# Kernel tuning notes

Hardware: AMD Instinct MI355X
Metric: run time of the kernel (lower is better)

## Reference

```python
import jax, jax.numpy as jnp
import numpy as np

NODE_N = 23
SEQ_LEN = 35
N_HEADS = 3
BN_EPS = 1e-5


def _normalize_digraph(A):
    # column-normalize: A @ diag(1/deg) (st-gcn tools.normalize_digraph)
    Dl = A.sum(0)
    inv = np.where(Dl > 0, 1.0 / np.where(Dl > 0, Dl, 1.0), 0.0)
    return A * inv[None, :]


def _build_A_ske():
    n = NODE_N
    bone = [[0, 2], [1, 2], [0, 3], [3, 6], [6, 9], [1, 4], [4, 7], [7, 10],
            [2, 5], [5, 8], [8, 12], [12, 15], [15, 17], [17, 19], [19, 21],
            [8, 13], [13, 16], [16, 18], [18, 20], [20, 22], [8, 11], [11, 14]]
    A_in = np.zeros((n, n), np.float64)
    A_out = np.zeros((n, n), np.float64)
    for i, j in bone:
        A_in[i, j] = 1.0
        A_out[j, i] = 1.0
    A_self = np.eye(n, dtype=np.float64)
    return np.stack([_normalize_digraph(A_in), _normalize_digraph(A_out), A_self]).astype(np.float32)


def setup_inputs() -> dict:
    key = jax.random.key(0)
    ks = jax.random.split(key, 12)
    b, c, o, n, l = 256, 64, 64, NODE_N, SEQ_LEN
    stdv = 1.0 / np.sqrt(n)           # reset_parameters: 1/sqrt(att.size(2)) = 1/sqrt(n)
    cbound = 1.0 / np.sqrt(c)         # conv2d 1x1 default init bound (fan_in = in_c)
    u = lambda k, shape, bnd: jax.random.uniform(k, shape, jnp.float32, -bnd, bnd)
    return {
        "x": jax.random.normal(ks[0], (b, c, n, l), jnp.float32),
        "cw1": u(ks[1], (N_HEADS, o, c), cbound),
        "cb1": u(ks[2], (N_HEADS, o), cbound),
        "cw2": u(ks[3], (N_HEADS, o, c), cbound),
        "cb2": u(ks[4], (N_HEADS, o), cbound),
        "bn_gamma": jnp.ones((N_HEADS, n * n), jnp.float32),
        "bn_beta": jnp.zeros((N_HEADS, n * n), jnp.float32),
        "mw": u(ks[5], (N_HEADS, o, c), cbound),
        "mb": u(ks[6], (N_HEADS, o), cbound),
        "att": jnp.full((N_HEADS, n, n), 1e-6, jnp.float32),
        "A_ske": jnp.asarray(_build_A_ske()),
        "weight_seq": u(ks[7], (l, l), stdv),
        "bias": u(ks[8], (l,), stdv),
    }


def reference(x, cw1, cb1, cw2, cb2, bn_gamma, bn_beta, mw, mb, att, A_ske, weight_seq, bias):
    b, c, n, l = x.shape
    o = cw1.shape[1]
    xp = jnp.transpose(x, (0, 1, 3, 2))                      # [b,c,l,n]

    # --- A_adp heads (vectorized across 3 heads) ---
    o1 = jnp.einsum('hoc,bcln->bholn', cw1, xp) + cb1[None, :, :, None, None]
    o2 = jnp.einsum('hoc,bcln->bholn', cw2, xp) + cb2[None, :, :, None, None]
    o1 = o1.reshape(b, N_HEADS, o * l, n)
    o2 = o2.reshape(b, N_HEADS, o * l, n)
    att_m = jnp.einsum('bhkm,bhkn->bhmn', o2, o1) / (o * l)  # [b,3,n,n]

    # BatchNorm1d over flattened n*n features, batch statistics (training mode)
    flat = att_m.reshape(b, N_HEADS, n * n)
    mean = flat.mean(axis=0)                                  # [3,n*n]
    var = flat.var(axis=0)                                    # biased, as torch BN
    flat = (flat - mean) / jnp.sqrt(var + BN_EPS) * bn_gamma + bn_beta
    A_adp = jax.nn.softmax(flat.reshape(b, N_HEADS, n, n), axis=-2)
    # dropout is identity in eval mode

    # --- graph convolution per head ---
    A = A_ske[None] + att[None] + A_adp                       # [b,3,n,n]
    support = jnp.einsum('bcln,bhnm->bhclm', xp, A)           # [b,3,c,l,n]
    head = jnp.einsum('hoc,bhclm->bholm', mw, support) + mb[None, :, :, None, None]
    gcn = jnp.transpose(head.sum(axis=1), (0, 1, 3, 2))       # [b,o,n,l]

    out = jnp.einsum('bonl,lm->bonm', gcn, weight_seq) + bias
    return out
```

## Files before the change

### kernel.cpp

```cpp
#include <hip/hip_runtime.h>
#include <hip/hip_bf16.h>

typedef __hip_bfloat16 bf16;
typedef __attribute__((ext_vector_type(8))) short bf16x8;
typedef __attribute__((ext_vector_type(4))) float f32x4;
typedef __attribute__((ext_vector_type(4))) unsigned short us4;
typedef __attribute__((ext_vector_type(8))) unsigned short us8;

#define NB   256
#define NN   23
#define NL   35
#define NNL  805
#define CNL  51520
#define NSQ  529
#define HF   1587
#define NCN  1472

#define OFF_W     0
#define OFF_U1    12288
#define OFF_U2    12480
#define OFF_S     12672
#define OFF_ATTM  12800
#define OFF_MEAN  419072
#define OFF_RSTD  420672
#define OFF_A     422272
#define OFF_MWH   828544
#define OFF_MWL   834688
#define OFF_MBS   840832
#define OFF_XTB   840960

__device__ inline unsigned short bfh(float x) {
    unsigned u = __float_as_uint(x);
    return (unsigned short)((u + 0x7FFFu + ((u >> 16) & 1u)) >> 16);
}
__device__ inline float bfh2f(unsigned short h) {
    return __uint_as_float(((unsigned)h) << 16);
}
__device__ inline unsigned short bf16rn(float x) {
    __hip_bfloat16 h = __float2bfloat16(x);
    return __builtin_bit_cast(unsigned short, h);
}

__global__ __launch_bounds__(512) void k_xt(const float* __restrict__ x,
                                            float* __restrict__ ws) {
    int b = blockIdx.x, ch = blockIdx.y, t = threadIdx.x;
    __shared__ float sx[16 * 805];
    const float* xb = x + b * CNL + ch * (16 * 805);
    unsigned short* xo = (unsigned short*)(ws + OFF_XTB) + (size_t)b * NL * 2944;
    for (int i = t; i < 16 * 805; i += 512) sx[i] = xb[i];
    __syncthreads();
    for (int item = t; item < 35 * 46; item += 512) {
        int l = item / 46, rem = item - l * 46;
        int n = rem >> 1, k2 = rem & 1;
        us8 hi, lo;
        #pragma unroll
        for (int e = 0; e < 8; e++) {
            float v = sx[(8 * k2 + e) * 805 + n * 35 + l];
            unsigned short hb = bfh(v);
            hi[e] = hb;
            lo[e] = bfh(v - bfh2f(hb));
        }
        unsigned short* dst = xo + (size_t)l * 2944 + n * 64 + 8 * (2 * ch + k2);
        *(us8*)(dst) = hi;
        *(us8*)(dst + 1472) = lo;
    }
}

__global__ __launch_bounds__(256) void k_prep(const float* __restrict__ cw1,
                                              const float* __restrict__ cb1,
                                              const float* __restrict__ cw2,
                                              const float* __restrict__ cb2,
                                              const float* __restrict__ mw,
                                              const float* __restrict__ mb,
                                              float* __restrict__ ws) {
    int h = blockIdx.x, t = threadIdx.x;
    __shared__ float s1[4096], s2[4096];
    if (h < 3) {
        for (int i = t; i < 4096; i += 256) {
            s1[i] = cw1[h * 4096 + i];
            s2[i] = cw2[h * 4096 + i];
        }
        __syncthreads();
        for (int i = t; i < 4096; i += 256) {
            int c2 = i >> 6, c1 = i & 63;
            float acc = 0.f;
            for (int o = 0; o < 64; o++) acc += s2[o * 64 + c2] * s1[o * 64 + c1];
            ws[OFF_W + h * 4096 + i] = acc;
        }
        if (t < 64) {
            float a = 0.f, b2 = 0.f;
            for (int o = 0; o < 64; o++) {
                a  += cb2[h * 64 + o] * s1[o * 64 + t];
                b2 += cb1[h * 64 + o] * s2[o * 64 + t];
            }
            ws[OFF_U1 + h * 64 + t] = a;
            ws[OFF_U2 + h * 64 + t] = b2;
        }
        if (t == 0) {
            float a = 0.f;
            for (int o = 0; o < 64; o++) a += cb1[h * 64 + o] * cb2[h * 64 + o];
            ws[OFF_S + h] = a;
        }
    } else {
        unsigned short* mh = (unsigned short*)(ws + OFF_MWH);
        unsigned short* ml = (unsigned short*)(ws + OFF_MWL);
        for (int i = t; i < 12288; i += 256) {
            float v = mw[i];
            unsigned short hb = bfh(v);
            mh[i] = hb;
            ml[i] = bfh(v - bfh2f(hb));
        }
        if (t < 64) ws[OFF_MBS + t] = mb[t] + mb[64 + t] + mb[128 + t];
    }
}

__global__ __launch_bounds__(256) void k_attm(float* __restrict__ ws) {
    const int b = blockIdx.x, h = blockIdx.y, t = threadIdx.x;
    const int lane = t & 63;
    const int w = __builtin_amdgcn_readfirstlane(t >> 6);
    const int lg = lane >> 4;
    const int lr = lane & 15;

    __shared__ unsigned short sXh[2][32 * 72];
    __shared__ unsigned short sXl[2][32 * 72];
    __shared__ unsigned short sPh[32 * 72];
    __shared__ unsigned short sPl[32 * 72];
    __shared__ float sxs[64 * 25];
    __shared__ float sA1[23], sA2[23];

    const unsigned short* xthl = (const unsigned short*)(ws + OFF_XTB);

    bf16x8 wh[2], wl[2];
    {
        const float* Wg = ws + OFF_W + h * 4096 + (16 * w + lr) * 64;
        #pragma unroll
        for (int s = 0; s < 2; s++) {
            const float* p = Wg + 32 * s + 8 * lg;
            float4 v0 = *(const float4*)(p);
            float4 v1 = *(const float4*)(p + 4);
            float vv[8] = {v0.x, v0.y, v0.z, v0.w, v1.x, v1.y, v1.z, v1.w};
            #pragma unroll
            for (int e = 0; e < 8; e++) {
                unsigned short hb = bfh(vv[e]);
                wh[s][e] = (short)hb;
                wl[s][e] = (short)bfh(vv[e] - bfh2f(hb));
            }
        }
    }

    const int j1 = t;
    const int p1 = j1 / 184, r1 = j1 - p1 * 184;
    const int n1 = r1 >> 3, k1 = r1 & 7;
    unsigned short* d1 = (p1 ? sXl[0] : sXh[0]) + n1 * 72 + 8 * k1;
    const int j2 = 256 + t;
    const int r2 = j2 - 184;
    const int n2 = r2 >> 3, k2 = r2 & 7;
    unsigned short* d2 = sXl[0] + n2 * 72 + 8 * k2;

    const int mt = w >> 1, nt = w & 1;
    f32x4 attC = {0.f, 0.f, 0.f, 0.f};
    float xa1[8] = {0, 0, 0, 0, 0, 0, 0, 0};
    float xa2[8] = {0, 0, 0, 0, 0, 0, 0, 0};

    {
        const us8* g = (const us8*)(xthl + (size_t)(b * NL) * 2944);
        us8 v1 = g[j1];
        *(us8*)(d1) = v1;
        #pragma unroll
        for (int e = 0; e < 8; e++) xa1[e] += bfh2f(v1[e]);
        if (t < 112) {
            us8 v2 = g[j2];
            *(us8*)(d2) = v2;
            #pragma unroll
            for (int e = 0; e < 8; e++) xa2[e] += bfh2f(v2[e]);
        }
    }

    #pragma unroll 1
    for (int l = 0; l < NL; l++) {
        const int cur = l & 1;
        __syncthreads();

        us8 vn1, vn2;
        if (l < NL - 1) {
            const us8* g = (const us8*)(xthl + (size_t)(b * NL + l + 1) * 2944);
            vn1 = g[j1];
            if (t < 112) vn2 = g[j2];
        }

        const unsigned short* xh = sXh[cur];
        const unsigned short* xl = sXl[cur];

        f32x4 pc[2];
        #pragma unroll
        for (int ntt = 0; ntt < 2; ntt++) {
            f32x4 c = {0.f, 0.f, 0.f, 0.f};
            #pragma unroll
            for (int s = 0; s < 2; s++) {
                int off = (ntt * 16 + lr) * 72 + 32 * s + 8 * lg;
                bf16x8 bh = *(const bf16x8*)(xh + off);
                bf16x8 bl = *(const bf16x8*)(xl + off);
                c = __builtin_amdgcn_mfma_f32_16x16x32_bf16(wh[s], bh, c, 0, 0, 0);
                c = __builtin_amdgcn_mfma_f32_16x16x32_bf16(wh[s], bl, c, 0, 0, 0);
                c = __builtin_amdgcn_mfma_f32_16x16x32_bf16(wl[s], bh, c, 0, 0, 0);
            }
            pc[ntt] = c;
        }
        #pragma unroll
        for (int ntt = 0; ntt < 2; ntt++) {
            int n = ntt * 16 + lr;
            int c2 = 16 * w + 4 * lg;
            us4 ph4, pl4;
            #pragma unroll
            for (int r = 0; r < 4; r++) {
                float v = pc[ntt][r];
                unsigned short hb = bf16rn(v);
                ph4[r] = hb;
                pl4[r] = bf16rn(v - bfh2f(hb));
            }
            *(us4*)(sPh + n * 72 + c2) = ph4;
            *(us4*)(sPl + n * 72 + c2) = pl4;
        }

        if (l < NL - 1) {
            *(us8*)(d1 + (cur ^ 1) * 2304) = vn1;
            #pragma unroll
            for (int e = 0; e < 8; e++) xa1[e] += bfh2f(vn1[e]);
            if (t < 112) {
                *(us8*)(d2 + (cur ^ 1) * 2304) = vn2;
                #pragma unroll
                for (int e = 0; e < 8; e++) xa2[e] += bfh2f(vn2[e]);
            }
        }
        __syncthreads();

        #pragma unroll
        for (int s = 0; s < 2; s++) {
            int aoff = (mt * 16 + lr) * 72 + 32 * s + 8 * lg;
            int boff = (nt * 16 + lr) * 72 + 32 * s + 8 * lg;
            bf16x8 ah = *(const bf16x8*)(xh + aoff);
            bf16x8 al = *(const bf16x8*)(xl + aoff);
            bf16x8 bh = *(const bf16x8*)(sPh + boff);
            bf16x8 bl = *(const bf16x8*)(sPl + boff);
            attC = __builtin_amdgcn_mfma_f32_16x16x32_bf16(ah, bh, attC, 0, 0, 0);
            attC = __builtin_amdgcn_mfma_f32_16x16x32_bf16(ah, bl, attC, 0, 0, 0);
            attC = __builtin_amdgcn_mfma_f32_16x16x32_bf16(al, bh, attC, 0, 0, 0);
        }
    }

    if (t < 184) {
        #pragma unroll
        for (int e = 0; e < 8; e++) sxs[(8 * k1 + e) * 25 + n1] = xa1[e];
    }
    __syncthreads();
    if (t >= 184) {
        #pragma unroll
        for (int e = 0; e < 8; e++) sxs[(8 * k1 + e) * 25 + n1] += xa1[e];
    }
    if (t < 112) {
        #pragma unroll
        for (int e = 0; e < 8; e++) sxs[(8 * k2 + e) * 25 + n2] += xa2[e];
    }
    __syncthreads();
    if (t < 23) {
        float a = 0.f;
        const float* u = ws + OFF_U1 + h * 64;
        for (int c = 0; c < 64; c++) a += u[c] * sxs[c * 25 + t];
        sA1[t] = a;
    } else if (t >= 32 && t < 55) {
        int n = t - 32;
        float a = 0.f;
        const float* u = ws + OFF_U2 + h * 64;
        for (int c = 0; c < 64; c++) a += u[c] * sxs[c * 25 + n];
        sA2[n] = a;
    }
    __syncthreads();

    float sh = ws[OFF_S + h];
    float* o = ws + OFF_ATTM + (size_t)b * HF + h * NSQ;
    int n = nt * 16 + lr;
    if (n < 23) {
        #pragma unroll
        for (int r = 0; r < 4; r++) {
            int m = mt * 16 + 4 * lg + r;
            if (m < 23)
                o[m * 23 + n] = (attC[r] + sA1[n] + sA2[m] + 35.f * sh) * (1.f / 2240.f);
        }
    }
}

__global__ __launch_bounds__(512) void k_bn(float* __restrict__ ws) {
    int t = threadIdx.x;
    int fi = t & 63, bg = t >> 6;
    int f = blockIdx.x * 64 + fi;
    __shared__ float rs[8][64], rs2[8][64];
    float s = 0.f, s2 = 0.f;
    if (f < HF) {
        const float* p = ws + OFF_ATTM + f + (size_t)bg * 32 * HF;
        for (int b = 0; b < 32; b++) {
            float v = p[b * HF];
            s += v; s2 += v * v;
        }
    }
    rs[bg][fi] = s; rs2[bg][fi] = s2;
    __syncthreads();
    if (bg == 0 && f < HF) {
        float ts = 0.f, ts2 = 0.f;
        #pragma unroll
        for (int g = 0; g < 8; g++) { ts += rs[g][fi]; ts2 += rs2[g][fi]; }
        float mean = ts * (1.f / 256.f);
        float var  = ts2 * (1.f / 256.f) - mean * mean;
        ws[OFF_MEAN + f] = mean;
        ws[OFF_RSTD + f] = rsqrtf(var + 1e-5f);
    }
}

__global__ __launch_bounds__(256) void k_adp(const float* __restrict__ gamma,
                                             const float* __restrict__ beta,
                                             const float* __restrict__ att,
                                             const float* __restrict__ aske,
                                             float* __restrict__ ws) {
    int b = blockIdx.x, h = blockIdx.y, t = threadIdx.x;
    __shared__ float sv[529];
    const float* am   = ws + OFF_ATTM + b * HF + h * NSQ;
    const float* mean = ws + OFF_MEAN + h * NSQ;
    const float* rstd = ws + OFF_RSTD + h * NSQ;
    for (int i = t; i < 529; i += 256) {
        sv[i] = (am[i] - mean[i]) * rstd[i] * gamma[h * NSQ + i] + beta[h * NSQ + i];
    }
    __syncthreads();
    if (t < 23) {
        float mx = -1e30f;
        #pragma unroll
        for (int m = 0; m < 23; m++) mx = fmaxf(mx, sv[m * 23 + t]);
        float e[23];
        float sum = 0.f;
        #pragma unroll
        for (int m = 0; m < 23; m++) {
            float v = __expf(sv[m * 23 + t] - mx);
            e[m] = v; sum += v;
        }
        float inv = 1.f / sum;
        #pragma unroll
        for (int m = 0; m < 23; m++) sv[m * 23 + t] = e[m] * inv;
    }
    __syncthreads();
    float* o = ws + OFF_A + b * HF + h * NSQ;
    for (int i = t; i < 529; i += 256) {
        o[i] = sv[i] + aske[h * NSQ + i] + att[h * NSQ + i];
    }
}

#define SYS 38
#define STS 44
__global__ __launch_bounds__(512, 2) void k_fused(float* __restrict__ ws,
                                                  const float* __restrict__ wseq,
                                                  const float* __restrict__ biasp,
                                                  float* __restrict__ out) {
    const int b = blockIdx.x, t = threadIdx.x;
    const int lane = t & 63;
    const int w = __builtin_amdgcn_readfirstlane(t >> 6);
    const int lg = lane >> 4, lr = lane & 15;
    const int nt = w >> 2, ot = w & 3;
    const int ot2 = w >> 1, mt = w & 1;

    __shared__ __align__(16) unsigned short sXh[32 * 72], sXl[32 * 72];
    __shared__ __align__(16) unsigned short sAT[3][2][32 * 40];
    __shared__ __align__(16) unsigned short sT[3][64 * STS];
    __shared__ __align__(16) unsigned short sY[1472 * SYS];
    __shared__ __align__(16) unsigned short sWTh[48 * 40], sWTl[48 * 40];
    __shared__ float sWt[3 * 35];
    __shared__ float sBias[35];

    const unsigned short* xthl = (const unsigned short*)(ws + OFF_XTB);
    const float* Ab  = ws + OFF_A + (size_t)b * HF;

    for (int i = t; i < 9 * 72; i += 512) {
        sXh[23 * 72 + i] = 0;
        sXl[23 * 72 + i] = 0;
    }
    for (int i = t; i < 3 * 1280; i += 512) {
        int h = i / 1280, r2 = i - h * 1280, m = r2 / 40, n = r2 - m * 40;
        float v = (n < 23 && m < 23) ? Ab[h * 529 + n * 23 + m] : 0.f;
        unsigned short hb = bfh(v);
        sAT[h][0][m * 40 + n] = hb;
        sAT[h][1][m * 40 + n] = bfh(v - bfh2f(hb));
    }
    for (int i = t; i < 48 * 40; i += 512) {
        int lp = i / 40, l = i - lp * 40;
        float v = (lp < 35 && l < 32) ? wseq[l * 35 + lp] : 0.f;
        unsigned short hb = bfh(v);
        sWTh[i] = hb;
        sWTl[i] = bfh(v - bfh2f(hb));
    }
    if (t < 105) sWt[t] = wseq[(32 + t / 35) * 35 + (t % 35)];
    if (t >= 128 && t < 163) sBias[t - 128] = biasp[t - 128];

    const unsigned short* mwh = (const unsigned short*)(ws + OFF_MWH);
    const unsigned short* mwl = (const unsigned short*)(ws + OFF_MWL);
    bf16x8 fwh[3][2], fwl[3][2];
    #pragma unroll
    for (int h = 0; h < 3; h++)
        #pragma unroll
        for (int s = 0; s < 2; s++) {
            int off = h * 4096 + (16 * ot + lr) * 64 + 32 * s + 8 * lg;
            fwh[h][s] = *(const bf16x8*)(mwh + off);
            fwl[h][s] = *(const bf16x8*)(mwl + off);
        }
    float4 mbsv = *(const float4*)(ws + OFF_MBS + 16 * ot2 + 4 * lg);
    float mb4[4] = {mbsv.x, mbsv.y, mbsv.z, mbsv.w};

    const int p1 = t / 184, r1 = t - p1 * 184;
    const int n1 = r1 >> 3, k1 = r1 & 7;
    unsigned short* d1 = (p1 ? sXl : sXh) + n1 * 72 + 8 * k1;

    const f32x4 zf = {0.f, 0.f, 0.f, 0.f};

    if (t < 368) {
        const us8* g = (const us8*)(xthl + (size_t)(b * NL) * 2944);
        *(us8*)d1 = g[t];
    }

    #pragma unroll 1
    for (int l = 0; l < NL; l++) {
        __syncthreads();

        us8 vn;
        if (l < NL - 1 && t < 368) {
            const us8* g = (const us8*)(xthl + (size_t)(b * NL + l + 1) * 2944);
            vn = g[t];
        }

        bf16x8 xh0 = *(const bf16x8*)(sXh + (16 * nt + lr) * 72 + 8 * lg);
        bf16x8 xh1 = *(const bf16x8*)(sXh + (16 * nt + lr) * 72 + 32 + 8 * lg);
        bf16x8 xl0 = *(const bf16x8*)(sXl + (16 * nt + lr) * 72 + 8 * lg);
        bf16x8 xl1 = *(const bf16x8*)(sXl + (16 * nt + lr) * 72 + 32 + 8 * lg);
        #pragma unroll
        for (int h = 0; h < 3; h++) {
            f32x4 cH = __builtin_amdgcn_mfma_f32_16x16x32_bf16(xh0, fwh[h][0], zf, 0, 0, 0);
            cH = __builtin_amdgcn_mfma_f32_16x16x32_bf16(xh1, fwh[h][1], cH, 0, 0, 0);
            f32x4 cC = __builtin_amdgcn_mfma_f32_16x16x32_bf16(xh0, fwl[h][0], zf, 0, 0, 0);
            cC = __builtin_amdgcn_mfma_f32_16x16x32_bf16(xh1, fwl[h][1], cC, 0, 0, 0);
            cC = __builtin_amdgcn_mfma_f32_16x16x32_bf16(xl0, fwh[h][0], cC, 0, 0, 0);
            cC = __builtin_amdgcn_mfma_f32_16x16x32_bf16(xl1, fwh[h][1], cC, 0, 0, 0);
            us4 t4;
            #pragma unroll
            for (int r = 0; r < 4; r++) t4[r] = bf16rn(cH[r] + cC[r]);
            *(us4*)(&sT[h][(16 * ot + lr) * STS + 16 * nt + 4 * lg]) = t4;
        }
        __syncthreads();

        f32x4 Yh = zf, Yc = zf;
        #pragma unroll
        for (int h = 0; h < 3; h++) {
            union { bf16x8 v; us4 q[2]; } tu;
            tu.q[0] = *(const us4*)(&sT[h][(16 * ot2 + lr) * STS + 8 * lg]);
            tu.q[1] = *(const us4*)(&sT[h][(16 * ot2 + lr) * STS + 8 * lg + 4]);
            bf16x8 ah = *(const bf16x8*)(&sAT[h][0][(16 * mt + lr) * 40 + 8 * lg]);
            bf16x8 al = *(const bf16x8*)(&sAT[h][1][(16 * mt + lr) * 40 + 8 * lg]);
            Yh = __builtin_amdgcn_mfma_f32_16x16x32_bf16(tu.v, ah, Yh, 0, 0, 0);
            Yc = __builtin_amdgcn_mfma_f32_16x16x32_bf16(tu.v, al, Yc, 0, 0, 0);
        }
        int m = 16 * mt + lr;
        if (m < 23) {
            #pragma unroll
            for (int r = 0; r < 4; r++) {
                int o = 16 * ot2 + 4 * lg + r;
                float yv = Yh[r] + Yc[r] + mb4[r];
                sY[(o * 23 + m) * SYS + l] = bf16rn(yv);
            }
        }

        if (l < NL - 1 && t < 368) *(us8*)d1 = vn;
    }
    __syncthreads();

    #pragma unroll 1
    for (int tt = w; tt < 276; tt += 8) {
        int pt = tt / 3, lt = tt - pt * 3;
        int pA = 16 * pt + lr;
        const unsigned short* yb = sY + pA * SYS + 8 * lg;
        union { bf16x8 v; unsigned u[4]; } au;
        au.u[0] = *(const unsigned*)(yb);
        au.u[1] = *(const unsigned*)(yb + 2);
        au.u[2] = *(const unsigned*)(yb + 4);
        au.u[3] = *(const unsigned*)(yb + 6);
        bf16x8 wbh = *(const bf16x8*)(sWTh + (16 * lt + lr) * 40 + 8 * lg);
        bf16x8 wbl = *(const bf16x8*)(sWTl + (16 * lt + lr) * 40 + 8 * lg);
        f32x4 c0 = __builtin_amdgcn_mfma_f32_16x16x32_bf16(au.v, wbh, zf, 0, 0, 0);
        f32x4 c1 = __builtin_amdgcn_mfma_f32_16x16x32_bf16(au.v, wbl, zf, 0, 0, 0);
        int lpc = 16 * lt + lr;
        if (lpc < 35) {
            float wt0 = sWt[lpc], wt1 = sWt[35 + lpc], wt2 = sWt[70 + lpc];
            float bv = sBias[lpc];
            #pragma unroll
            for (int r = 0; r < 4; r++) {
                int pr = 16 * pt + 4 * lg + r;
                const unsigned short* yt = sY + pr * SYS + 32;
                unsigned t0 = *(const unsigned*)(yt);
                unsigned t1 = *(const unsigned*)(yt + 2);
                float v = c0[r] + c1[r] + bv
                        + bfh2f((unsigned short)(t0 & 0xffff)) * wt0
                        + bfh2f((unsigned short)(t0 >> 16))    * wt1
                        + bfh2f((unsigned short)(t1 & 0xffff)) * wt2;
                out[((size_t)b * 1472 + pr) * 35 + lpc] = v;
            }
        }
    }
}

extern "C" void kernel_launch(void* const* d_in, const int* in_sizes, int n_in,
                              void* d_out, int out_size, void* d_ws, size_t ws_size,
                              hipStream_t stream) {
    const float* x    = (const float*)d_in[0];
    const float* cw1  = (const float*)d_in[1];
    const float* cb1  = (const float*)d_in[2];
    const float* cw2  = (const float*)d_in[3];
    const float* cb2  = (const float*)d_in[4];
    const float* gam  = (const float*)d_in[5];
    const float* bet  = (const float*)d_in[6];
    const float* mw   = (const float*)d_in[7];
    const float* mb   = (const float*)d_in[8];
    const float* att  = (const float*)d_in[9];
    const float* aske = (const float*)d_in[10];
    const float* wsq  = (const float*)d_in[11];
    const float* bias = (const float*)d_in[12];
    float* ws = (float*)d_ws;
    float* out = (float*)d_out;

    hipLaunchKernelGGL(k_prep, dim3(4),       dim3(256),  0, stream, cw1, cb1, cw2, cb2, mw, mb, ws);
    hipLaunchKernelGGL(k_xt,   dim3(256, 4),  dim3(512),  0, stream, x, ws);
    hipLaunchKernelGGL(k_attm, dim3(256, 3),  dim3(256),  0, stream, ws);
    hipLaunchKernelGGL(k_bn,   dim3(25),      dim3(512),  0, stream, ws);
    hipLaunchKernelGGL(k_adp,  dim3(256, 3),  dim3(256),  0, stream, gam, bet, att, aske, ws);
    hipLaunchKernelGGL(k_fused, dim3(256),    dim3(512),  0, stream, ws, wsq, bias, out);
}
```

Baseline: 264.5 us.

## Software-pipeline attm loop with triple-buffered X and double-buffered P

Restructures the k_attm time loop so that the projection (phase A) for step l+1 runs alongside the attention accumulation (phase B) for step l. This drops one of the two __syncthreads per iteration, using a 3-slot X buffer and a 2-slot P buffer, and prefetches two steps ahead. It also wraps MFMA sections in s_setprio in both kernels to favour matrix issue. The cost is more LDS, which may lower occupancy, plus extra modulo indexing.

```diff
diff --git a/kernel.cpp b/kernel.cpp
--- a/kernel.cpp
+++ b/kernel.cpp
@@ -121,10 +121,10 @@
     const int lg = lane >> 4;
     const int lr = lane & 15;
 
-    __shared__ unsigned short sXh[2][32 * 72];
-    __shared__ unsigned short sXl[2][32 * 72];
-    __shared__ unsigned short sPh[32 * 72];
-    __shared__ unsigned short sPl[32 * 72];
+    __shared__ unsigned short sXh[3][32 * 72];
+    __shared__ unsigned short sXl[3][32 * 72];
+    __shared__ unsigned short sPh[2][32 * 72];
+    __shared__ unsigned short sPl[2][32 * 72];
     __shared__ float sxs[64 * 25];
     __shared__ float sA1[23], sA2[23];
 
@@ -162,91 +162,108 @@
     float xa1[8] = {0, 0, 0, 0, 0, 0, 0, 0};
     float xa2[8] = {0, 0, 0, 0, 0, 0, 0, 0};
 
-    {
-        const us8* g = (const us8*)(xthl + (size_t)(b * NL) * 2944);
+#define PHASE_A(LA)                                                            \
+    {                                                                          \
+        const int slA = (LA) % 3;                                              \
+        const int pbA = (LA) & 1;                                              \
+        const unsigned short* xhA = sXh[slA];                                  \
+        const unsigned short* xlA = sXl[slA];                                  \
+        f32x4 pcA[2];                                                          \
+        _Pragma("unroll")                                                      \
+        for (int ntt = 0; ntt < 2; ntt++) {                                    \
+            f32x4 c = {0.f, 0.f, 0.f, 0.f};                                    \
+            _Pragma("unroll")                                                  \
+            for (int s = 0; s < 2; s++) {                                      \
+                int off = (ntt * 16 + lr) * 72 + 32 * s + 8 * lg;              \
+                bf16x8 bh = *(const bf16x8*)(xhA + off);                       \
+                bf16x8 bl = *(const bf16x8*)(xlA + off);                       \
+                c = __builtin_amdgcn_mfma_f32_16x16x32_bf16(wh[s], bh, c, 0, 0, 0); \
+                c = __builtin_amdgcn_mfma_f32_16x16x32_bf16(wh[s], bl, c, 0, 0, 0); \
+                c = __builtin_amdgcn_mfma_f32_16x16x32_bf16(wl[s], bh, c, 0, 0, 0); \
+            }                                                                  \
+            pcA[ntt] = c;                                                      \
+        }                                                                      \
+        _Pragma("unroll")                                                      \
+        for (int ntt = 0; ntt < 2; ntt++) {                                    \
+            int n = ntt * 16 + lr;                                             \
+            int c2 = 16 * w + 4 * lg;                                          \
+            us4 ph4, pl4;                                                      \
+            _Pragma("unroll")                                                  \
+            for (int r = 0; r < 4; r++) {                                      \
+                float v = pcA[ntt][r];                                         \
+                unsigned short hb = bf16rn(v);                                 \
+                ph4[r] = hb;                                                   \
+                pl4[r] = bf16rn(v - bfh2f(hb));                                \
+            }                                                                  \
+            *(us4*)(sPh[pbA] + n * 72 + c2) = ph4;                             \
+            *(us4*)(sPl[pbA] + n * 72 + c2) = pl4;                             \
+        }                                                                      \
+    }
+
+#define PHASE_B(L)                                                             \
+    {                                                                          \
+        const int slB = (L) % 3;                                               \
+        const int pbB = (L) & 1;                                               \
+        const unsigned short* xhB = sXh[slB];                                  \
+        const unsigned short* xlB = sXl[slB];                                  \
+        _Pragma("unroll")                                                      \
+        for (int s = 0; s < 2; s++) {                                          \
+            int aoff = (mt * 16 + lr) * 72 + 32 * s + 8 * lg;                  \
+            int boff = (nt * 16 + lr) * 72 + 32 * s + 8 * lg;                  \
+            bf16x8 ah = *(const bf16x8*)(xhB + aoff);                          \
+            bf16x8 al = *(const bf16x8*)(xlB + aoff);                          \
+            bf16x8 bh = *(const bf16x8*)(sPh[pbB] + boff);                     \
+            bf16x8 bl = *(const bf16x8*)(sPl[pbB] + boff);                     \
+            attC = __builtin_amdgcn_mfma_f32_16x16x32_bf16(ah, bh, attC, 0, 0, 0); \
+            attC = __builtin_amdgcn_mfma_f32_16x16x32_bf16(ah, bl, attC, 0, 0, 0); \
+            attC = __builtin_amdgcn_mfma_f32_16x16x32_bf16(al, bh, attC, 0, 0, 0); \
+        }                                                                      \
+    }
+
+    #pragma unroll
+    for (int l0 = 0; l0 < 2; l0++) {
+        const us8* g = (const us8*)(xthl + (size_t)(b * NL + l0) * 2944);
         us8 v1 = g[j1];
-        *(us8*)(d1) = v1;
+        *(us8*)(d1 + l0 * 2304) = v1;
         #pragma unroll
         for (int e = 0; e < 8; e++) xa1[e] += bfh2f(v1[e]);
         if (t < 112) {
             us8 v2 = g[j2];
-            *(us8*)(d2) = v2;
+            *(us8*)(d2 + l0 * 2304) = v2;
             #pragma unroll
             for (int e = 0; e < 8; e++) xa2[e] += bfh2f(v2[e]);
         }
     }
+    __syncthreads();
+    PHASE_A(0)
 
     #pragma unroll 1
     for (int l = 0; l < NL; l++) {
-        const int cur = l & 1;
-        __syncthreads();
-
         us8 vn1, vn2;
-        if (l < NL - 1) {
-            const us8* g = (const us8*)(xthl + (size_t)(b * NL + l + 1) * 2944);
+        if (l + 2 < NL) {
+            const us8* g = (const us8*)(xthl + (size_t)(b * NL + l + 2) * 2944);
             vn1 = g[j1];
             if (t < 112) vn2 = g[j2];
         }
-
-        const unsigned short* xh = sXh[cur];
-        const unsigned short* xl = sXl[cur];
-
-        f32x4 pc[2];
-        #pragma unroll
-        for (int ntt = 0; ntt < 2; ntt++) {
-            f32x4 c = {0.f, 0.f, 0.f, 0.f};
-            #pragma unroll
-            for (int s = 0; s < 2; s++) {
-                int off = (ntt * 16 + lr) * 72 + 32 * s + 8 * lg;
-                bf16x8 bh = *(const bf16x8*)(xh + off);
-                bf16x8 bl = *(const bf16x8*)(xl + off);
-                c = __builtin_amdgcn_mfma_f32_16x16x32_bf16(wh[s], bh, c, 0, 0, 0);
-                c = __builtin_amdgcn_mfma_f32_16x16x32_bf16(wh[s], bl, c, 0, 0, 0);
-                c = __builtin_amdgcn_mfma_f32_16x16x32_bf16(wl[s], bh, c, 0, 0, 0);
-            }
-            pc[ntt] = c;
-        }
-        #pragma unroll
-        for (int ntt = 0; ntt < 2; ntt++) {
-            int n = ntt * 16 + lr;
-            int c2 = 16 * w + 4 * lg;
-            us4 ph4, pl4;
-            #pragma unroll
-            for (int r = 0; r < 4; r++) {
-                float v = pc[ntt][r];
-                unsigned short hb = bf16rn(v);
-                ph4[r] = hb;
-                pl4[r] = bf16rn(v - bfh2f(hb));
-            }
-            *(us4*)(sPh + n * 72 + c2) = ph4;
-            *(us4*)(sPl + n * 72 + c2) = pl4;
-        }
-
-        if (l < NL - 1) {
-            *(us8*)(d1 + (cur ^ 1) * 2304) = vn1;
+        __syncthreads();
+        __builtin_amdgcn_s_setprio(1);
+        if (l + 1 < NL) PHASE_A(l + 1)
+        PHASE_B(l)
+        __builtin_amdgcn_s_setprio(0);
+        if (l + 2 < NL) {
+            int sl2o = ((l + 2) % 3) * 2304;
+            *(us8*)(d1 + sl2o) = vn1;
             #pragma unroll
             for (int e = 0; e < 8; e++) xa1[e] += bfh2f(vn1[e]);
             if (t < 112) {
-                *(us8*)(d2 + (cur ^ 1) * 2304) = vn2;
+                *(us8*)(d2 + sl2o) = vn2;
                 #pragma unroll
                 for (int e = 0; e < 8; e++) xa2[e] += bfh2f(vn2[e]);
             }
         }
-        __syncthreads();
-
-        #pragma unroll
-        for (int s = 0; s < 2; s++) {
-            int aoff = (mt * 16 + lr) * 72 + 32 * s + 8 * lg;
-            int boff = (nt * 16 + lr) * 72 + 32 * s + 8 * lg;
-            bf16x8 ah = *(const bf16x8*)(xh + aoff);
-            bf16x8 al = *(const bf16x8*)(xl + aoff);
-            bf16x8 bh = *(const bf16x8*)(sPh + boff);
-            bf16x8 bl = *(const bf16x8*)(sPl + boff);
-            attC = __builtin_amdgcn_mfma_f32_16x16x32_bf16(ah, bh, attC, 0, 0, 0);
-            attC = __builtin_amdgcn_mfma_f32_16x16x32_bf16(ah, bl, attC, 0, 0, 0);
-            attC = __builtin_amdgcn_mfma_f32_16x16x32_bf16(al, bh, attC, 0, 0, 0);
-        }
-    }
+    }
+#undef PHASE_A
+#undef PHASE_B
 
     if (t < 184) {
         #pragma unroll
@@ -435,6 +452,7 @@
         bf16x8 xh1 = *(const bf16x8*)(sXh + (16 * nt + lr) * 72 + 32 + 8 * lg);
         bf16x8 xl0 = *(const bf16x8*)(sXl + (16 * nt + lr) * 72 + 8 * lg);
         bf16x8 xl1 = *(const bf16x8*)(sXl + (16 * nt + lr) * 72 + 32 + 8 * lg);
+        __builtin_amdgcn_s_setprio(1);
         #pragma unroll
         for (int h = 0; h < 3; h++) {
             f32x4 cH = __builtin_amdgcn_mfma_f32_16x16x32_bf16(xh0, fwh[h][0], zf, 0, 0, 0);
@@ -448,9 +466,11 @@
             for (int r = 0; r < 4; r++) t4[r] = bf16rn(cH[r] + cC[r]);
             *(us4*)(&sT[h][(16 * ot + lr) * STS + 16 * nt + 4 * lg]) = t4;
         }
+        __builtin_amdgcn_s_setprio(0);
         __syncthreads();
 
         f32x4 Yh = zf, Yc = zf;
+        __builtin_amdgcn_s_setprio(1);
         #pragma unroll
         for (int h = 0; h < 3; h++) {
             union { bf16x8 v; us4 q[2]; } tu;
@@ -461,6 +481,7 @@
             Yh = __builtin_amdgcn_mfma_f32_16x16x32_bf16(tu.v, ah, Yh, 0, 0, 0);
             Yc = __builtin_amdgcn_mfma_f32_16x16x32_bf16(tu.v, al, Yc, 0, 0, 0);
         }
+        __builtin_amdgcn_s_setprio(0);
         int m = 16 * mt + lr;
         if (m < 23) {
             #pragma unroll
```

Measured after the change: 261.3 us. About the same (-1.2%).
